# Kernel optimization log

Hardware: AMD Instinct MI355X
Metric: run time of the kernel (lower is better)

Reference implementation:

```python
import jax, jax.numpy as jnp
import numpy as np

N_NODES = 100000
N_EDGES = 3200000
N_FEAT = 512
N_HIDS = [256, 128]
N_CLASS = 40


def _glorot(key, shape):
    # matches common GraphConvolution init scale (uniform in +-1/sqrt(fan_out))
    stdv = 1.0 / np.sqrt(shape[-1])
    return jax.random.uniform(key, shape, jnp.float32, -stdv, stdv)


def setup_inputs() -> dict:
    key = jax.random.key(0)
    ks = jax.random.split(key, 16)
    x = jax.random.normal(ks[0], (N_NODES, N_FEAT), jnp.float32)
    edge_src = jax.random.randint(ks[1], (N_EDGES,), 0, N_NODES, jnp.int32)
    edge_dst = jax.random.randint(ks[2], (N_EDGES,), 0, N_NODES, jnp.int32)
    edge_val = jax.random.uniform(ks[3], (N_EDGES,), jnp.float32)
    dims = [N_FEAT] + N_HIDS + [N_CLASS]
    inp = {"x": x, "edge_src": edge_src, "edge_dst": edge_dst, "edge_val": edge_val}
    for i in range(len(dims) - 1):
        inp[f"W{i}"] = _glorot(ks[4 + 2 * i], (dims[i], dims[i + 1]))
        inp[f"b{i}"] = _glorot(ks[5 + 2 * i], (dims[i + 1],))
    return inp


def _spmm(edge_src, edge_dst, edge_val, s):
    # (sparse adj) @ s via gather + segment-sum over destination nodes
    msgs = edge_val[:, None] * s[edge_src]  # [E, d]
    return jax.ops.segment_sum(msgs, edge_dst, num_segments=N_NODES)


def reference(x, edge_src, edge_dst, edge_val, W0, b0, W1, b1, W2, b2):
    Ws = [W0, W1, W2]
    bs = [b0, b1, b2]
    h = x
    for i in range(len(Ws) - 1):
        s = h @ Ws[i] + bs[i]
        h = jax.nn.relu(_spmm(edge_src, edge_dst, edge_val, s))
        # dropout: identity in eval mode (training=False)
    s = h @ Ws[-1] + bs[-1]
    logits = _spmm(edge_src, edge_dst, edge_val, s)
    return jax.nn.log_softmax(logits, axis=1)
```

## Files before the change

### kernel.cpp

```cpp
#include <hip/hip_runtime.h>
#include <hip/hip_bf16.h>
#include <math.h>

#define N_NODES 100000
#define N_EDGES 3200000
#define NBUK 782
#define BCAP 4800
#define EPB 12500

typedef __hip_bfloat16 bf16_t;
typedef __attribute__((ext_vector_type(8))) short bf16x8;
typedef __attribute__((ext_vector_type(4))) float floatx4;
typedef __attribute__((ext_vector_type(2))) float f32x2;

__device__ inline float2 bf2_to_f2(unsigned u) {
  float2 f;
  f.x = __uint_as_float(u << 16);
  f.y = __uint_as_float(u & 0xffff0000u);
  return f;
}
__device__ inline unsigned f2_to_bf2(float x, float y) {
  unsigned ux = __float_as_uint(x);
  unsigned uy = __float_as_uint(y);
  unsigned bx = (ux + 0x7fffu + ((ux >> 16) & 1u)) >> 16;
  unsigned by = (uy + 0x7fffu + ((uy >> 16) & 1u)) & 0xffff0000u;
  return bx | by;
}
__device__ inline unsigned f_to_bf1(float x) {
  unsigned u = __float_as_uint(x);
  return (u + 0x7fffu + ((u >> 16) & 1u)) >> 16;
}
__device__ inline unsigned relu_bf2(unsigned u) {
  unsigned lo = (u & 0x8000u) ? 0u : (u & 0xFFFFu);
  unsigned hi = (u & 0x80000000u) ? 0u : (u & 0xFFFF0000u);
  return lo | hi;
}

__global__ __launch_bounds__(256) void bucket_hist_kernel(
    const int* __restrict__ edst, int* __restrict__ cntp) {
  __shared__ int h[NBUK];
  for (int i = threadIdx.x; i < NBUK; i += 256) h[i] = 0;
  __syncthreads();
  int start = blockIdx.x * 4096;
  int end = start + 4096 < N_EDGES ? start + 4096 : N_EDGES;
  for (int i = start + threadIdx.x; i < end; i += 256)
    atomicAdd(&h[edst[i] >> 7], 1);
  __syncthreads();
  for (int i = threadIdx.x; i < NBUK; i += 256)
    if (h[i]) atomicAdd(&cntp[i << 4], h[i]);
}

__global__ __launch_bounds__(1024) void scan_buckets_kernel(
    const int* __restrict__ cntp, int* __restrict__ base,
    int* __restrict__ cursorp, int* __restrict__ rowptr) {
  __shared__ int sc[1024];
  int t = threadIdx.x;
  int v = (t < NBUK) ? cntp[t << 4] : 0;
  sc[t] = v;
  __syncthreads();
  #pragma unroll
  for (int off = 1; off < 1024; off <<= 1) {
    int u = (t >= off) ? sc[t - off] : 0;
    __syncthreads();
    sc[t] += u;
    __syncthreads();
  }
  int ex = sc[t] - v;
  if (t < NBUK) { base[t] = ex; cursorp[t << 4] = ex; }
  if (t == NBUK - 1) base[NBUK] = ex + v;
  if (t == 0) rowptr[N_NODES] = N_EDGES;
}

__global__ __launch_bounds__(256) void staged_scatter_kernel(
    const int* __restrict__ esrc, const int* __restrict__ edst,
    const float* __restrict__ eval, int* __restrict__ cursorp,
    int2* __restrict__ tmp) {
  __shared__ int h[NBUK];
  __shared__ int gb[NBUK];
  const int tid = threadIdx.x;
  const int start = blockIdx.x * EPB;
  const int end = start + EPB < N_EDGES ? start + EPB : N_EDGES;
  for (int i = tid; i < NBUK; i += 256) h[i] = 0;
  __syncthreads();
  for (int e = start + tid; e < end; e += 256)
    atomicAdd(&h[edst[e] >> 7], 1);
  __syncthreads();
  for (int i = tid; i < NBUK; i += 256) {
    int c = h[i];
    gb[i] = c ? atomicAdd(&cursorp[i << 4], c) : 0;
    h[i] = 0;
  }
  __syncthreads();
  for (int e = start + tid; e < end; e += 256) {
    int d = edst[e];
    int b = d >> 7;
    int r = atomicAdd(&h[b], 1);
    tmp[gb[b] + r] =
        make_int2(esrc[e] | ((d & 127) << 17), __float_as_int(eval[e]));
  }
}

__global__ __launch_bounds__(256) void sort_bucket_kernel(
    const int* __restrict__ base, const int2* __restrict__ tmp,
    int2* __restrict__ csr, int* __restrict__ rowptr) {
  __shared__ int2 ebuf[BCAP];
  __shared__ int bin[128], sc[128], cur[128];
  const int b = blockIdx.x, tid = threadIdx.x;
  const int bbase = base[b], bend = base[b + 1];
  const int bcnt = bend - bbase;
  if (tid < 128) bin[tid] = 0;
  __syncthreads();
  for (int i = tid; i < bcnt; i += 256) {
    int2 e = tmp[bbase + i];
    if (i < BCAP) ebuf[i] = e;
    atomicAdd(&bin[(e.x >> 17) & 127], 1);
  }
  __syncthreads();
  if (tid < 128) sc[tid] = bin[tid];
  __syncthreads();
  #pragma unroll
  for (int off = 1; off < 128; off <<= 1) {
    int u = (tid < 128 && tid >= off) ? sc[tid - off] : 0;
    __syncthreads();
    if (tid < 128) sc[tid] += u;
    __syncthreads();
  }
  if (tid < 128) {
    int ex = sc[tid] - bin[tid];
    int node = (b << 7) + tid;
    if (node < N_NODES) rowptr[node] = bbase + ex;
    cur[tid] = ex;
  }
  __syncthreads();
  for (int i = tid; i < bcnt; i += 256) {
    int2 e = (i < BCAP) ? ebuf[i] : tmp[bbase + i];
    int d = (e.x >> 17) & 127;
    int p = atomicAdd(&cur[d], 1);
    csr[bbase + p] = make_int2(e.x & 0x1FFFF, e.y);
  }
}

__global__ __launch_bounds__(256) void transpose_w_kernel(
    const float* __restrict__ W, unsigned short* __restrict__ Wt,
    int ksh, int N) {
  int idx = blockIdx.x * 256 + threadIdx.x;
  int K = 1 << ksh;
  if (idx >= N * K) return;
  int n = idx >> ksh;
  int k = idx & (K - 1);
  Wt[idx] = (unsigned short)f_to_bf1(W[(size_t)k * N + n]);
}

template<bool AFP32, bool RELU, bool OF8>
__global__ __launch_bounds__(256) void mfma_gemm_kernel(
    const void* __restrict__ Xv, const unsigned short* __restrict__ Wt,
    const float* __restrict__ bias, void* __restrict__ out,
    int M, int K, int N, int ldo) {
  constexpr int BM = 128, BN = 128, BK = 32, LDSTR = 40;
  __shared__ __align__(16) unsigned short a_lds[BM * LDSTR];
  __shared__ __align__(16) unsigned short b_lds[BN * LDSTR];

  const int tid = threadIdx.x;
  const int lane = tid & 63;
  const int wave = tid >> 6;
  const int q = lane >> 4;
  const int r16 = lane & 15;
  const int wm = (wave >> 1) * 64;
  const int wn = (wave & 1) * 64;
  const int bm = blockIdx.x * BM;
  const int bn = blockIdx.y * BN;

  floatx4 acc[4][4] = {};

  for (int k0 = 0; k0 < K; k0 += BK) {
    if (AFP32) {
      const float* X = (const float*)Xv;
      #pragma unroll
      for (int i = 0; i < 4; ++i) {
        int c = tid + i * 256;
        int row = c >> 3, kc = (c & 7) * 4;
        float4 v = make_float4(0.f, 0.f, 0.f, 0.f);
        if (bm + row < M)
          v = *(const float4*)(X + (size_t)(bm + row) * K + k0 + kc);
        unsigned lo = f2_to_bf2(v.x, v.y);
        unsigned hi = f2_to_bf2(v.z, v.w);
        *(uint2*)&a_lds[row * LDSTR + kc] = make_uint2(lo, hi);
      }
    } else {
      const unsigned short* X = (const unsigned short*)Xv;
      #pragma unroll
      for (int i = 0; i < 2; ++i) {
        int c = tid + i * 256;
        int row = c >> 2, kc = (c & 3) * 8;
        uint4 v = make_uint4(0u, 0u, 0u, 0u);
        if (bm + row < M)
          v = *(const uint4*)(X + (size_t)(bm + row) * K + k0 + kc);
        if (RELU) {
          v.x = relu_bf2(v.x); v.y = relu_bf2(v.y);
          v.z = relu_bf2(v.z); v.w = relu_bf2(v.w);
        }
        *(uint4*)&a_lds[row * LDSTR + kc] = v;
      }
    }
    #pragma unroll
    for (int i = 0; i < 2; ++i) {
      int c = tid + i * 256;
      int row = c >> 2, kc = (c & 3) * 8;
      uint4 v = make_uint4(0u, 0u, 0u, 0u);
      if (bn + row < N)
        v = *(const uint4*)(Wt + (size_t)(bn + row) * K + k0 + kc);
      *(uint4*)&b_lds[row * LDSTR + kc] = v;
    }
    __syncthreads();

    bf16x8 af[4], bfr[4];
    #pragma unroll
    for (int t = 0; t < 4; ++t)
      af[t] = *(const bf16x8*)&a_lds[(wm + t * 16 + r16) * LDSTR + q * 8];
    #pragma unroll
    for (int t = 0; t < 4; ++t)
      bfr[t] = *(const bf16x8*)&b_lds[(wn + t * 16 + r16) * LDSTR + q * 8];
    #pragma unroll
    for (int mi = 0; mi < 4; ++mi)
      #pragma unroll
      for (int ni = 0; ni < 4; ++ni)
        acc[mi][ni] = __builtin_amdgcn_mfma_f32_16x16x32_bf16(
            af[mi], bfr[ni], acc[mi][ni], 0, 0, 0);
    __syncthreads();
  }

  #pragma unroll
  for (int ni = 0; ni < 4; ++ni) {
    int col = bn + wn + ni * 16 + r16;
    float bv = (col < N) ? bias[col] : 0.f;
    #pragma unroll
    for (int mi = 0; mi < 4; ++mi) {
      #pragma unroll
      for (int r = 0; r < 4; ++r) {
        int row = bm + wm + mi * 16 + q * 4 + r;
        float v = acc[mi][ni][r] + bv;
        if (OF8) {
          float vo = __shfl_xor(v, 1);
          int pk = __builtin_amdgcn_cvt_pk_fp8_f32(v, vo, 0, false);
          int pk2 = __shfl_xor(pk, 2);
          unsigned four = ((unsigned)pk & 0xFFFFu) | ((unsigned)pk2 << 16);
          if (((lane & 3) == 0) && row < M && col < N) {
            *(unsigned*)((unsigned char*)out + (size_t)row * ldo + col) = four;
          }
        } else {
          int bits = (int)f_to_bf1(v);
          int other = __shfl_xor(bits, 1);
          if (((lane & 1) == 0) && row < M && col < N) {
            *(unsigned*)((unsigned short*)out + (size_t)row * ldo + col) =
                (unsigned)bits | ((unsigned)other << 16);
          }
        }
      }
    }
  }
}

__global__ __launch_bounds__(256) void spmm256f8_kernel(
    const int* __restrict__ rowptr, const int2* __restrict__ csr,
    const unsigned char* __restrict__ s, bf16_t* __restrict__ h) {
  int node = blockIdx.x * 4 + (threadIdx.x >> 6);
  int lane = threadIdx.x & 63;
  if (node >= N_NODES) return;
  int beg = rowptr[node], end = rowptr[node + 1];
  float4 a0 = make_float4(0.f, 0.f, 0.f, 0.f);
  float4 a1 = a0, a2 = a0, a3 = a0;
  int i = beg;
  for (; i + 4 <= end; i += 4) {
    int2 e0 = csr[i + 0], e1 = csr[i + 1], e2 = csr[i + 2], e3 = csr[i + 3];
    unsigned r0 = *((const unsigned*)(s + (size_t)e0.x * 256) + lane);
    unsigned r1 = *((const unsigned*)(s + (size_t)e1.x * 256) + lane);
    unsigned r2 = *((const unsigned*)(s + (size_t)e2.x * 256) + lane);
    unsigned r3 = *((const unsigned*)(s + (size_t)e3.x * 256) + lane);
    float v0 = __int_as_float(e0.y);
    f32x2 l0 = __builtin_amdgcn_cvt_pk_f32_fp8((int)r0, false);
    f32x2 h0 = __builtin_amdgcn_cvt_pk_f32_fp8((int)r0, true);
    a0.x += v0 * l0[0]; a0.y += v0 * l0[1];
    a0.z += v0 * h0[0]; a0.w += v0 * h0[1];
    float v1 = __int_as_float(e1.y);
    f32x2 l1 = __builtin_amdgcn_cvt_pk_f32_fp8((int)r1, false);
    f32x2 h1 = __builtin_amdgcn_cvt_pk_f32_fp8((int)r1, true);
    a1.x += v1 * l1[0]; a1.y += v1 * l1[1];
    a1.z += v1 * h1[0]; a1.w += v1 * h1[1];
    float v2 = __int_as_float(e2.y);
    f32x2 l2 = __builtin_amdgcn_cvt_pk_f32_fp8((int)r2, false);
    f32x2 h2 = __builtin_amdgcn_cvt_pk_f32_fp8((int)r2, true);
    a2.x += v2 * l2[0]; a2.y += v2 * l2[1];
    a2.z += v2 * h2[0]; a2.w += v2 * h2[1];
    float v3 = __int_as_float(e3.y);
    f32x2 l3 = __builtin_amdgcn_cvt_pk_f32_fp8((int)r3, false);
    f32x2 h3 = __builtin_amdgcn_cvt_pk_f32_fp8((int)r3, true);
    a3.x += v3 * l3[0]; a3.y += v3 * l3[1];
    a3.z += v3 * h3[0]; a3.w += v3 * h3[1];
  }
  for (; i < end; ++i) {
    int2 e = csr[i];
    unsigned r = *((const unsigned*)(s + (size_t)e.x * 256) + lane);
    float v = __int_as_float(e.y);
    f32x2 lo = __builtin_amdgcn_cvt_pk_f32_fp8((int)r, false);
    f32x2 hi = __builtin_amdgcn_cvt_pk_f32_fp8((int)r, true);
    a0.x += v * lo[0]; a0.y += v * lo[1];
    a0.z += v * hi[0]; a0.w += v * hi[1];
  }
  float4 acc;
  acc.x = (a0.x + a1.x) + (a2.x + a3.x);
  acc.y = (a0.y + a1.y) + (a2.y + a3.y);
  acc.z = (a0.z + a1.z) + (a2.z + a3.z);
  acc.w = (a0.w + a1.w) + (a2.w + a3.w);
  uint2 o = make_uint2(f2_to_bf2(acc.x, acc.y), f2_to_bf2(acc.z, acc.w));
  *((uint2*)(h + (size_t)node * 256) + lane) = o;
}

__global__ __launch_bounds__(256) void spmm128f8_kernel(
    const int* __restrict__ rowptr, const int2* __restrict__ csr,
    const unsigned char* __restrict__ s, bf16_t* __restrict__ h) {
  int node = blockIdx.x * 8 + (threadIdx.x >> 5);
  int l = threadIdx.x & 31;
  if (node >= N_NODES) return;
  int beg = rowptr[node], end = rowptr[node + 1];
  float4 a0 = make_float4(0.f, 0.f, 0.f, 0.f);
  float4 a1 = a0, a2 = a0, a3 = a0;
  int i = beg;
  for (; i + 4 <= end; i += 4) {
    int2 e0 = csr[i + 0], e1 = csr[i + 1], e2 = csr[i + 2], e3 = csr[i + 3];
    unsigned r0 = *((const unsigned*)(s + (size_t)e0.x * 128) + l);
    unsigned r1 = *((const unsigned*)(s + (size_t)e1.x * 128) + l);
    unsigned r2 = *((const unsigned*)(s + (size_t)e2.x * 128) + l);
    unsigned r3 = *((const unsigned*)(s + (size_t)e3.x * 128) + l);
    float v0 = __int_as_float(e0.y);
    f32x2 l0 = __builtin_amdgcn_cvt_pk_f32_fp8((int)r0, false);
    f32x2 h0 = __builtin_amdgcn_cvt_pk_f32_fp8((int)r0, true);
    a0.x += v0 * l0[0]; a0.y += v0 * l0[1];
    a0.z += v0 * h0[0]; a0.w += v0 * h0[1];
    float v1 = __int_as_float(e1.y);
    f32x2 l1 = __builtin_amdgcn_cvt_pk_f32_fp8((int)r1, false);
    f32x2 h1 = __builtin_amdgcn_cvt_pk_f32_fp8((int)r1, true);
    a1.x += v1 * l1[0]; a1.y += v1 * l1[1];
    a1.z += v1 * h1[0]; a1.w += v1 * h1[1];
    float v2 = __int_as_float(e2.y);
    f32x2 l2 = __builtin_amdgcn_cvt_pk_f32_fp8((int)r2, false);
    f32x2 h2 = __builtin_amdgcn_cvt_pk_f32_fp8((int)r2, true);
    a2.x += v2 * l2[0]; a2.y += v2 * l2[1];
    a2.z += v2 * h2[0]; a2.w += v2 * h2[1];
    float v3 = __int_as_float(e3.y);
    f32x2 l3 = __builtin_amdgcn_cvt_pk_f32_fp8((int)r3, false);
    f32x2 h3 = __builtin_amdgcn_cvt_pk_f32_fp8((int)r3, true);
    a3.x += v3 * l3[0]; a3.y += v3 * l3[1];
    a3.z += v3 * h3[0]; a3.w += v3 * h3[1];
  }
  for (; i < end; ++i) {
    int2 e = csr[i];
    unsigned r = *((const unsigned*)(s + (size_t)e.x * 128) + l);
    float v = __int_as_float(e.y);
    f32x2 lo = __builtin_amdgcn_cvt_pk_f32_fp8((int)r, false);
    f32x2 hi = __builtin_amdgcn_cvt_pk_f32_fp8((int)r, true);
    a0.x += v * lo[0]; a0.y += v * lo[1];
    a0.z += v * hi[0]; a0.w += v * hi[1];
  }
  float4 acc;
  acc.x = (a0.x + a1.x) + (a2.x + a3.x);
  acc.y = (a0.y + a1.y) + (a2.y + a3.y);
  acc.z = (a0.z + a1.z) + (a2.z + a3.z);
  acc.w = (a0.w + a1.w) + (a2.w + a3.w);
  uint2 o = make_uint2(f2_to_bf2(acc.x, acc.y), f2_to_bf2(acc.z, acc.w));
  *((uint2*)(h + (size_t)node * 128) + l) = o;
}

__global__ __launch_bounds__(256) void spmm40_kernel(
    const int* __restrict__ rowptr, const int2* __restrict__ csr,
    const bf16_t* __restrict__ s, float* __restrict__ out) {
  int node = blockIdx.x * 8 + (threadIdx.x >> 5);
  int l = threadIdx.x & 31;
  if (node >= N_NODES) return;
  bool active = (l < 20);
  int beg = rowptr[node], end = rowptr[node + 1];
  float2 a0 = make_float2(0.f, 0.f), a1 = a0, a2 = a0, a3 = a0;
  int i = beg;
  for (; i + 4 <= end; i += 4) {
    int2 e0 = csr[i + 0], e1 = csr[i + 1], e2 = csr[i + 2], e3 = csr[i + 3];
    unsigned r0 = active ? *((const unsigned*)(s + (size_t)e0.x * 64) + l) : 0u;
    unsigned r1 = active ? *((const unsigned*)(s + (size_t)e1.x * 64) + l) : 0u;
    unsigned r2 = active ? *((const unsigned*)(s + (size_t)e2.x * 64) + l) : 0u;
    unsigned r3 = active ? *((const unsigned*)(s + (size_t)e3.x * 64) + l) : 0u;
    float v0 = __int_as_float(e0.y);
    float2 f0 = bf2_to_f2(r0);
    a0.x += v0 * f0.x; a0.y += v0 * f0.y;
    float v1 = __int_as_float(e1.y);
    float2 f1 = bf2_to_f2(r1);
    a1.x += v1 * f1.x; a1.y += v1 * f1.y;
    float v2 = __int_as_float(e2.y);
    float2 f2 = bf2_to_f2(r2);
    a2.x += v2 * f2.x; a2.y += v2 * f2.y;
    float v3 = __int_as_float(e3.y);
    float2 f3 = bf2_to_f2(r3);
    a3.x += v3 * f3.x; a3.y += v3 * f3.y;
  }
  for (; i < end; ++i) {
    int2 e = csr[i];
    unsigned r = active ? *((const unsigned*)(s + (size_t)e.x * 64) + l) : 0u;
    float v = __int_as_float(e.y);
    float2 f = bf2_to_f2(r);
    a0.x += v * f.x; a0.y += v * f.y;
  }
  float2 acc;
  acc.x = (a0.x + a1.x) + (a2.x + a3.x);
  acc.y = (a0.y + a1.y) + (a2.y + a3.y);
  if (active) *((float2*)(out + (size_t)node * 40) + l) = acc;
}

__global__ __launch_bounds__(256) void logsoftmax_kernel(float* __restrict__ io,
                                                         int M) {
  const int lane = threadIdx.x & 63;
  const int row = blockIdx.x * 4 + (threadIdx.x >> 6);
  if (row >= M) return;
  float v = (lane < 40) ? io[(size_t)row * 40 + lane] : -INFINITY;
  float m = v;
  #pragma unroll
  for (int off = 32; off > 0; off >>= 1)
    m = fmaxf(m, __shfl_xor(m, off));
  float ex = (lane < 40) ? __expf(v - m) : 0.f;
  float sum = ex;
  #pragma unroll
  for (int off = 32; off > 0; off >>= 1)
    sum += __shfl_xor(sum, off);
  if (lane < 40) io[(size_t)row * 40 + lane] = v - m - logf(sum);
}

extern "C" void kernel_launch(void* const* d_in, const int* in_sizes, int n_in,
                              void* d_out, int out_size, void* d_ws,
                              size_t ws_size, hipStream_t stream) {
  const float* x    = (const float*)d_in[0];
  const int*   esrc = (const int*)d_in[1];
  const int*   edst = (const int*)d_in[2];
  const float* eval = (const float*)d_in[3];
  const float* W0   = (const float*)d_in[4];
  const float* b0   = (const float*)d_in[5];
  const float* W1   = (const float*)d_in[6];
  const float* b1   = (const float*)d_in[7];
  const float* W2   = (const float*)d_in[8];
  const float* b2   = (const float*)d_in[9];
  float* out = (float*)d_out;

  char* ws = (char*)d_ws;
  unsigned char* bufA = (unsigned char*)(ws + 0);
  bf16_t* bufB    = (bf16_t*)(ws + 51200000);
  int2*   csr     = (int2*)  (ws + 102400000);
  int2*   tmp     = (int2*)  (ws + 128000000);
  int*    rowptr  = (int*)   (ws + 153600000);
  int*    cntp    = (int*)   (ws + 154004480);
  int*    cursorp = (int*)   (ws + 154058752);
  int*    base    = (int*)   (ws + 154112000);
  unsigned short* Wt0 = (unsigned short*)(ws + 154120192);
  unsigned short* Wt1 = (unsigned short*)(ws + 154390528);
  unsigned short* Wt2 = (unsigned short*)(ws + 154460160);

  const int M = N_NODES;
  dim3 blk(256);

  hipMemsetAsync(cntp, 0, NBUK * 64, stream);
  bucket_hist_kernel<<<NBUK, blk, 0, stream>>>(edst, cntp);
  scan_buckets_kernel<<<1, 1024, 0, stream>>>(cntp, base, cursorp, rowptr);
  staged_scatter_kernel<<<(N_EDGES + EPB - 1) / EPB, blk, 0, stream>>>(
      esrc, edst, eval, cursorp, tmp);
  sort_bucket_kernel<<<NBUK, blk, 0, stream>>>(base, tmp, csr, rowptr);

  transpose_w_kernel<<<(512 * 256 + 255) / 256, blk, 0, stream>>>(W0, Wt0, 9, 256);
  transpose_w_kernel<<<(256 * 128 + 255) / 256, blk, 0, stream>>>(W1, Wt1, 8, 128);
  transpose_w_kernel<<<(128 * 40 + 255) / 256, blk, 0, stream>>>(W2, Wt2, 7, 40);

  const int MB = (M + 127) / 128;

  mfma_gemm_kernel<true, false, true><<<dim3(MB, 2), blk, 0, stream>>>(
      x, Wt0, b0, bufA, M, 512, 256, 256);
  spmm256f8_kernel<<<25000, blk, 0, stream>>>(rowptr, csr, bufA, bufB);

  mfma_gemm_kernel<false, true, true><<<dim3(MB, 1), blk, 0, stream>>>(
      bufB, Wt1, b1, bufA, M, 256, 128, 128);
  spmm128f8_kernel<<<12500, blk, 0, stream>>>(rowptr, csr, bufA, bufB);

  mfma_gemm_kernel<false, true, false><<<dim3(MB, 1), blk, 0, stream>>>(
      bufB, Wt2, b2, bufA, M, 128, 40, 64);
  spmm40_kernel<<<12500, blk, 0, stream>>>(rowptr, csr, (const bf16_t*)bufA, out);

  logsoftmax_kernel<<<25000, blk, 0, stream>>>(out, M);
}
```

Before: 966.4 us.

## Double-buffer LDS tiles in MFMA GEMM with register prefetch of next K slice

```diff
diff --git a/kernel.cpp b/kernel.cpp
--- a/kernel.cpp
+++ b/kernel.cpp
@@ -151,14 +151,73 @@
   Wt[idx] = (unsigned short)f_to_bf1(W[(size_t)k * N + n]);
 }
 
+#define GEMM_ISSUE(k0)                                                      \
+  if (AFP32) {                                                              \
+    const float* X = (const float*)Xv;                                      \
+    _Pragma("unroll") for (int i = 0; i < 4; ++i) {                         \
+      int c = tid + i * 256;                                                \
+      int row = c >> 3, kc = (c & 7) * 4;                                   \
+      fa[i] = make_float4(0.f, 0.f, 0.f, 0.f);                              \
+      if (bm + row < M)                                                     \
+        fa[i] = *(const float4*)(X + (size_t)(bm + row) * K + (k0) + kc);   \
+    }                                                                       \
+  } else {                                                                  \
+    const unsigned short* X = (const unsigned short*)Xv;                    \
+    _Pragma("unroll") for (int i = 0; i < 2; ++i) {                         \
+      int c = tid + i * 256;                                                \
+      int row = c >> 2, kc = (c & 3) * 8;                                   \
+      va[i] = make_uint4(0u, 0u, 0u, 0u);                                   \
+      if (bm + row < M)                                                     \
+        va[i] = *(const uint4*)(X + (size_t)(bm + row) * K + (k0) + kc);    \
+    }                                                                       \
+  }                                                                         \
+  {                                                                         \
+    _Pragma("unroll") for (int i = 0; i < 2; ++i) {                         \
+      int c = tid + i * 256;                                                \
+      int row = c >> 2, kc = (c & 3) * 8;                                   \
+      vb[i] = make_uint4(0u, 0u, 0u, 0u);                                   \
+      if (bn + row < N)                                                     \
+        vb[i] = *(const uint4*)(Wt + (size_t)(bn + row) * K + (k0) + kc);   \
+    }                                                                       \
+  }
+
+#define GEMM_WRITE(buf)                                                     \
+  if (AFP32) {                                                              \
+    _Pragma("unroll") for (int i = 0; i < 4; ++i) {                         \
+      int c = tid + i * 256;                                                \
+      int row = c >> 3, kc = (c & 7) * 4;                                   \
+      unsigned lo = f2_to_bf2(fa[i].x, fa[i].y);                            \
+      unsigned hi = f2_to_bf2(fa[i].z, fa[i].w);                            \
+      *(uint2*)&a_lds[buf][row * LDSTR + kc] = make_uint2(lo, hi);          \
+    }                                                                       \
+  } else {                                                                  \
+    _Pragma("unroll") for (int i = 0; i < 2; ++i) {                         \
+      int c = tid + i * 256;                                                \
+      int row = c >> 2, kc = (c & 3) * 8;                                   \
+      uint4 v = va[i];                                                      \
+      if (RELU) {                                                           \
+        v.x = relu_bf2(v.x); v.y = relu_bf2(v.y);                           \
+        v.z = relu_bf2(v.z); v.w = relu_bf2(v.w);                           \
+      }                                                                     \
+      *(uint4*)&a_lds[buf][row * LDSTR + kc] = v;                           \
+    }                                                                       \
+  }                                                                         \
+  {                                                                         \
+    _Pragma("unroll") for (int i = 0; i < 2; ++i) {                         \
+      int c = tid + i * 256;                                                \
+      int row = c >> 2, kc = (c & 3) * 8;                                   \
+      *(uint4*)&b_lds[buf][row * LDSTR + kc] = vb[i];                       \
+    }                                                                       \
+  }
+
 template<bool AFP32, bool RELU, bool OF8>
 __global__ __launch_bounds__(256) void mfma_gemm_kernel(
     const void* __restrict__ Xv, const unsigned short* __restrict__ Wt,
     const float* __restrict__ bias, void* __restrict__ out,
     int M, int K, int N, int ldo) {
   constexpr int BM = 128, BN = 128, BK = 32, LDSTR = 40;
-  __shared__ __align__(16) unsigned short a_lds[BM * LDSTR];
-  __shared__ __align__(16) unsigned short b_lds[BN * LDSTR];
+  __shared__ __align__(16) unsigned short a_lds[2][BM * LDSTR];
+  __shared__ __align__(16) unsigned short b_lds[2][BN * LDSTR];
 
   const int tid = threadIdx.x;
   const int lane = tid & 63;
@@ -171,62 +230,38 @@
   const int bn = blockIdx.y * BN;
 
   floatx4 acc[4][4] = {};
-
+  float4 fa[4];
+  uint4 va[2];
+  uint4 vb[2];
+
+  GEMM_ISSUE(0);
+  GEMM_WRITE(0);
+  __syncthreads();
+
+  int cur = 0;
   for (int k0 = 0; k0 < K; k0 += BK) {
-    if (AFP32) {
-      const float* X = (const float*)Xv;
-      #pragma unroll
-      for (int i = 0; i < 4; ++i) {
-        int c = tid + i * 256;
-        int row = c >> 3, kc = (c & 7) * 4;
-        float4 v = make_float4(0.f, 0.f, 0.f, 0.f);
-        if (bm + row < M)
-          v = *(const float4*)(X + (size_t)(bm + row) * K + k0 + kc);
-        unsigned lo = f2_to_bf2(v.x, v.y);
-        unsigned hi = f2_to_bf2(v.z, v.w);
-        *(uint2*)&a_lds[row * LDSTR + kc] = make_uint2(lo, hi);
-      }
-    } else {
-      const unsigned short* X = (const unsigned short*)Xv;
-      #pragma unroll
-      for (int i = 0; i < 2; ++i) {
-        int c = tid + i * 256;
-        int row = c >> 2, kc = (c & 3) * 8;
-        uint4 v = make_uint4(0u, 0u, 0u, 0u);
-        if (bm + row < M)
-          v = *(const uint4*)(X + (size_t)(bm + row) * K + k0 + kc);
-        if (RELU) {
-          v.x = relu_bf2(v.x); v.y = relu_bf2(v.y);
-          v.z = relu_bf2(v.z); v.w = relu_bf2(v.w);
-        }
-        *(uint4*)&a_lds[row * LDSTR + kc] = v;
-      }
-    }
-    #pragma unroll
-    for (int i = 0; i < 2; ++i) {
-      int c = tid + i * 256;
-      int row = c >> 2, kc = (c & 3) * 8;
-      uint4 v = make_uint4(0u, 0u, 0u, 0u);
-      if (bn + row < N)
-        v = *(const uint4*)(Wt + (size_t)(bn + row) * K + k0 + kc);
-      *(uint4*)&b_lds[row * LDSTR + kc] = v;
-    }
-    __syncthreads();
+    const bool more = (k0 + BK) < K;
+    if (more) { GEMM_ISSUE(k0 + BK); }
 
     bf16x8 af[4], bfr[4];
     #pragma unroll
     for (int t = 0; t < 4; ++t)
-      af[t] = *(const bf16x8*)&a_lds[(wm + t * 16 + r16) * LDSTR + q * 8];
+      af[t] = *(const bf16x8*)&a_lds[cur][(wm + t * 16 + r16) * LDSTR + q * 8];
     #pragma unroll
     for (int t = 0; t < 4; ++t)
-      bfr[t] = *(const bf16x8*)&b_lds[(wn + t * 16 + r16) * LDSTR + q * 8];
+      bfr[t] = *(const bf16x8*)&b_lds[cur][(wn + t * 16 + r16) * LDSTR + q * 8];
     #pragma unroll
     for (int mi = 0; mi < 4; ++mi)
       #pragma unroll
       for (int ni = 0; ni < 4; ++ni)
         acc[mi][ni] = __builtin_amdgcn_mfma_f32_16x16x32_bf16(
             af[mi], bfr[ni], acc[mi][ni], 0, 0, 0);
-    __syncthreads();
+
+    if (more) {
+      GEMM_WRITE(cur ^ 1);
+      __syncthreads();
+      cur ^= 1;
+    }
   }
 
   #pragma unroll
```

Result: slower. 990.9 us (+2.5%).

## Double-buffer GEMM tiles with direct global-to-LDS loads and swizzled layout

Applied to the files above, without the earlier changes.

```diff
diff --git a/kernel.cpp b/kernel.cpp
--- a/kernel.cpp
+++ b/kernel.cpp
@@ -35,6 +35,16 @@
   unsigned hi = (u & 0x80000000u) ? 0u : (u & 0xFFFF0000u);
   return lo | hi;
 }
+__device__ inline bf16x8 u4_to_bf8(uint4 v) {
+  union { uint4 u; bf16x8 b; } c;
+  c.u = v;
+  return c.b;
+}
+
+#define GLOAD16(gp, lp)                                                        \
+  __builtin_amdgcn_global_load_lds(                                            \
+      (const __attribute__((address_space(1))) unsigned int*)(const void*)(gp),\
+      (__attribute__((address_space(3))) unsigned int*)(void*)(lp), 16, 0, 0)
 
 __global__ __launch_bounds__(256) void bucket_hist_kernel(
     const int* __restrict__ edst, int* __restrict__ cntp) {
@@ -156,9 +166,12 @@
     const void* __restrict__ Xv, const unsigned short* __restrict__ Wt,
     const float* __restrict__ bias, void* __restrict__ out,
     int M, int K, int N, int ldo) {
-  constexpr int BM = 128, BN = 128, BK = 32, LDSTR = 40;
-  __shared__ __align__(16) unsigned short a_lds[BM * LDSTR];
-  __shared__ __align__(16) unsigned short b_lds[BN * LDSTR];
+  constexpr int BM = 128, BN = 128, BK = 32;
+  constexpr int ABUF = BM * BK * (AFP32 ? 4 : 2);
+  constexpr int BBUF = BN * BK * 2;
+  __shared__ __align__(16) char lds[2 * ABUF + 2 * BBUF];
+  char* const a0 = lds;
+  char* const b0 = lds + 2 * ABUF;
 
   const int tid = threadIdx.x;
   const int lane = tid & 63;
@@ -172,61 +185,86 @@
 
   floatx4 acc[4][4] = {};
 
-  for (int k0 = 0; k0 < K; k0 += BK) {
-    if (AFP32) {
+  auto stage = [&](int buf, int k0) {
+    if constexpr (AFP32) {
       const float* X = (const float*)Xv;
       #pragma unroll
-      for (int i = 0; i < 4; ++i) {
-        int c = tid + i * 256;
-        int row = c >> 3, kc = (c & 7) * 4;
-        float4 v = make_float4(0.f, 0.f, 0.f, 0.f);
-        if (bm + row < M)
-          v = *(const float4*)(X + (size_t)(bm + row) * K + k0 + kc);
-        unsigned lo = f2_to_bf2(v.x, v.y);
-        unsigned hi = f2_to_bf2(v.z, v.w);
-        *(uint2*)&a_lds[row * LDSTR + kc] = make_uint2(lo, hi);
+      for (int j = 0; j < 4; ++j) {
+        int chunk = (wave * 4 + j) * 64 + lane;
+        int row = chunk >> 3, slot = chunk & 7;
+        int g = slot ^ (row & 7);
+        int rowc = (bm + row < M) ? bm + row : M - 1;
+        const float* gp = X + (size_t)rowc * K + k0 + g * 4;
+        GLOAD16(gp, a0 + buf * ABUF + chunk * 16);
       }
     } else {
       const unsigned short* X = (const unsigned short*)Xv;
       #pragma unroll
-      for (int i = 0; i < 2; ++i) {
-        int c = tid + i * 256;
-        int row = c >> 2, kc = (c & 3) * 8;
-        uint4 v = make_uint4(0u, 0u, 0u, 0u);
-        if (bm + row < M)
-          v = *(const uint4*)(X + (size_t)(bm + row) * K + k0 + kc);
-        if (RELU) {
-          v.x = relu_bf2(v.x); v.y = relu_bf2(v.y);
-          v.z = relu_bf2(v.z); v.w = relu_bf2(v.w);
-        }
-        *(uint4*)&a_lds[row * LDSTR + kc] = v;
+      for (int j = 0; j < 2; ++j) {
+        int chunk = (wave * 2 + j) * 64 + lane;
+        int row = chunk >> 2, slot = chunk & 3;
+        int g = slot ^ ((row >> 1) & 3);
+        int rowc = (bm + row < M) ? bm + row : M - 1;
+        const unsigned short* gp = X + (size_t)rowc * K + k0 + g * 8;
+        GLOAD16(gp, a0 + buf * ABUF + chunk * 16);
       }
     }
     #pragma unroll
-    for (int i = 0; i < 2; ++i) {
-      int c = tid + i * 256;
-      int row = c >> 2, kc = (c & 3) * 8;
-      uint4 v = make_uint4(0u, 0u, 0u, 0u);
-      if (bn + row < N)
-        v = *(const uint4*)(Wt + (size_t)(bn + row) * K + k0 + kc);
-      *(uint4*)&b_lds[row * LDSTR + kc] = v;
+    for (int j = 0; j < 2; ++j) {
+      int chunk = (wave * 2 + j) * 64 + lane;
+      int row = chunk >> 2, slot = chunk & 3;
+      int g = slot ^ ((row >> 1) & 3);
+      int rowc = (bn + row < N) ? bn + row : N - 1;
+      const unsigned short* gp = Wt + (size_t)rowc * K + k0 + g * 8;
+      GLOAD16(gp, b0 + buf * BBUF + chunk * 16);
     }
-    __syncthreads();
+  };
+
+  stage(0, 0);
+  __syncthreads();
+
+  int cur = 0;
+  for (int k0 = 0; k0 < K; k0 += BK) {
+    if (k0 + BK < K) stage(cur ^ 1, k0 + BK);
 
     bf16x8 af[4], bfr[4];
     #pragma unroll
-    for (int t = 0; t < 4; ++t)
-      af[t] = *(const bf16x8*)&a_lds[(wm + t * 16 + r16) * LDSTR + q * 8];
+    for (int t = 0; t < 4; ++t) {
+      int row = wm + t * 16 + r16;
+      if constexpr (AFP32) {
+        const char* base = a0 + cur * ABUF + row * 128;
+        int p = row & 7;
+        float4 c0 = *(const float4*)(base + (((2 * q) ^ p) * 16));
+        float4 c1 = *(const float4*)(base + (((2 * q + 1) ^ p) * 16));
+        uint4 u = make_uint4(f2_to_bf2(c0.x, c0.y), f2_to_bf2(c0.z, c0.w),
+                             f2_to_bf2(c1.x, c1.y), f2_to_bf2(c1.z, c1.w));
+        af[t] = u4_to_bf8(u);
+      } else {
+        int slot = q ^ ((row >> 1) & 3);
+        uint4 u = *(const uint4*)(a0 + cur * ABUF + row * 64 + slot * 16);
+        if (RELU) {
+          u.x = relu_bf2(u.x); u.y = relu_bf2(u.y);
+          u.z = relu_bf2(u.z); u.w = relu_bf2(u.w);
+        }
+        af[t] = u4_to_bf8(u);
+      }
+    }
     #pragma unroll
-    for (int t = 0; t < 4; ++t)
-      bfr[t] = *(const bf16x8*)&b_lds[(wn + t * 16 + r16) * LDSTR + q * 8];
+    for (int t = 0; t < 4; ++t) {
+      int row = wn + t * 16 + r16;
+      int slot = q ^ ((row >> 1) & 3);
+      uint4 u = *(const uint4*)(b0 + cur * BBUF + row * 64 + slot * 16);
+      bfr[t] = u4_to_bf8(u);
+    }
     #pragma unroll
     for (int mi = 0; mi < 4; ++mi)
       #pragma unroll
       for (int ni = 0; ni < 4; ++ni)
         acc[mi][ni] = __builtin_amdgcn_mfma_f32_16x16x32_bf16(
             af[mi], bfr[ni], acc[mi][ni], 0, 0, 0);
+
     __syncthreads();
+    cur ^= 1;
   }
 
   #pragma unroll
```

Result: faster. 914.6 us (-5.4%).
